# Kernel optimization log

Measured on AMD Instinct MI355X. Metric: run time of the kernel, lower is better.

The kernel has to match this reference:

```python
import jax, jax.numpy as jnp
import numpy as np

R, N, E = 3, 50000, 800000
IN, HID, HEADS, OUT = 128, 64, 2, 64


def setup_inputs() -> dict:
    key = jax.random.key(0)
    ks = jax.random.split(key, 12)
    s = 0.05
    return {
        "x": jax.random.normal(ks[0], (N, IN), jnp.float32),
        "src": jax.random.randint(ks[1], (R, E), 0, N, jnp.int32),
        "dst": jax.random.randint(ks[2], (R, E), 0, N, jnp.int32),
        "W1": jax.random.normal(ks[3], (R, IN, HEADS * HID), jnp.float32) * s,
        "al1": jax.random.normal(ks[4], (R, HEADS, HID), jnp.float32) * s,
        "ar1": jax.random.normal(ks[5], (R, HEADS, HID), jnp.float32) * s,
        "b1": jnp.zeros((R, HEADS * HID), jnp.float32),
        "W2": jax.random.normal(ks[6], (R, HEADS * HID, HID), jnp.float32) * s,
        "al2": jax.random.normal(ks[7], (R, 1, HID), jnp.float32) * s,
        "ar2": jax.random.normal(ks[8], (R, 1, HID), jnp.float32) * s,
        "b2": jnp.zeros((R, HID), jnp.float32),
        "Wl": jax.random.normal(ks[9], (HID, OUT), jnp.float32) * s,
        "bl": jnp.zeros((OUT,), jnp.float32),
    }


def gat_conv(x, src, dst, W, al, ar, b, heads, dim):
    """DGL GATConv on a homogeneous edge list: returns elu(aggregated) [N, heads, dim]."""
    n = x.shape[0]
    feat = (x @ W).reshape(n, heads, dim)                     # [N,H,D]
    el = (feat * al).sum(-1)                                  # [N,H]
    er = (feat * ar).sum(-1)                                  # [N,H]
    e = jax.nn.leaky_relu(el[src] + er[dst], 0.2)             # [E,H]
    # segment softmax over incoming edges of each dst node
    m = jax.lax.stop_gradient(jax.ops.segment_max(e, dst, num_segments=n))
    ee = jnp.exp(e - m[dst])                                  # [E,H]
    z = jax.ops.segment_sum(ee, dst, num_segments=n)          # [N,H]
    a = ee / z[dst]                                           # [E,H]
    msg = feat[src] * a[..., None]                            # [E,H,D]
    out = jax.ops.segment_sum(msg, dst, num_segments=n)       # [N,H,D]
    return jax.nn.elu(out + b.reshape(1, heads, dim))


def reference(x, src, dst, W1, al1, ar1, b1, W2, al2, ar2, b2, Wl, bl):
    # layer 1: per-relation GATConv, summed (HeteroGraphConv default aggregate='sum')
    h1 = sum(gat_conv(x, src[r], dst[r], W1[r], al1[r], ar1[r], b1[r], HEADS, HID)
             for r in range(R))                               # [N,H,HID]
    h1 = h1.reshape(N, HEADS * HID)                           # flatten(1)
    # layer 2: single-head GATConv per relation, summed
    h2 = sum(gat_conv(h1, src[r], dst[r], W2[r], al2[r], ar2[r], b2[r], 1, HID)
             for r in range(R))                               # [N,1,HID]
    h2 = h2.mean(1)                                           # mean over the single head
    return h2 @ Wl + bl                                       # [N,OUT]
```

## Files before the change

kernel.cpp:

```cpp
#include <hip/hip_runtime.h>

constexpr int R = 3;
constexpr int N = 50000;
constexpr int E = 800000;
constexpr int K = 128;
constexpr int NT16 = N / 16;
constexpr int GB = (NT16 + 3) / 4;

constexpr int BKT_SH = 9;
constexpr int NBKT = (N + 511) >> 9;
constexpr int BCAP = 10240;
constexpr int P1E = 4096;
constexpr int P1B = (E + P1E - 1) / P1E;

constexpr int NF1 = 192;
constexpr int NF2 = 96;
constexpr int NF3 = 16;
constexpr int PREP_BLKS = (NF1 + NF2 + NF3) / 4;

typedef __attribute__((ext_vector_type(8))) short bf16x8;
typedef __attribute__((ext_vector_type(4))) float f32x4;
typedef __attribute__((ext_vector_type(2))) float f32x2;


__device__ inline unsigned short f2bf(float f) {
    unsigned u = __float_as_uint(f);
    u += 0x7FFF + ((u >> 16) & 1);
    return (unsigned short)(u >> 16);
}
__device__ inline float bf2f_lo(unsigned p) { return __uint_as_float(p << 16); }
__device__ inline float bf2f_hi(unsigned p) { return __uint_as_float(p & 0xFFFF0000u); }

__device__ inline float lrelu02(float x) { return fmaxf(x, 0.2f * x); }
__device__ inline float elu1f(float x) { return x > 0.f ? x : __expf(x) - 1.f; }


__device__ void prep_frag(int f, int lane,
                          const float* __restrict__ W1, const float* __restrict__ W2,
                          const float* __restrict__ Wl,
                          short* __restrict__ WF1, short* __restrict__ WF2,
                          short* __restrict__ WF3) {
    int c = lane & 15, g = lane >> 4;
    const float* srcp;
    int stride;
    short* dstp;
    int hl;
    if (f < NF1) {
        hl = f & 1;
        int h = (f >> 1) & 1, ks = (f >> 2) & 3, tr = (f >> 4) & 3, r = f >> 6;
        int col = h * 64 + tr * 16 + c;
        srcp = W1 + (size_t)r * 128 * 128 + (size_t)(ks * 32 + g * 8) * 128 + col;
        stride = 128;
        dstp = WF1 + (size_t)f * 512 + lane * 8;
    } else if (f < NF1 + NF2) {
        int f2 = f - NF1;
        hl = f2 & 1;
        int ks = (f2 >> 1) & 3, t = f2 >> 3;
        int c192 = t * 16 + c;
        int r = c192 >> 6, col64 = c192 & 63;
        srcp = W2 + (size_t)r * 128 * 64 + (size_t)(ks * 32 + g * 8) * 64 + col64;
        stride = 64;
        dstp = WF2 + (size_t)f2 * 512 + lane * 8;
    } else {
        int f3 = f - NF1 - NF2;
        hl = f3 & 1;
        int ks = (f3 >> 1) & 1, t = f3 >> 2;
        srcp = Wl + (size_t)(ks * 32 + g * 8) * 64 + t * 16 + c;
        stride = 64;
        dstp = WF3 + (size_t)f3 * 512 + lane * 8;
    }
#pragma unroll
    for (int i = 0; i < 8; i++) {
        float v = srcp[(size_t)i * stride];
        unsigned short hi = f2bf(v);
        dstp[i] = hl ? (short)f2bf(v - __uint_as_float(((unsigned)hi) << 16)) : (short)hi;
    }
}

__global__ __launch_bounds__(256) void fusedA(const int* __restrict__ src,
                                              const int* __restrict__ dst,
                                              int* __restrict__ gcur,
                                              uint2* __restrict__ ebuf,
                                              const float* __restrict__ W1,
                                              const float* __restrict__ W2,
                                              const float* __restrict__ Wl,
                                              short* __restrict__ WF1,
                                              short* __restrict__ WF2,
                                              short* __restrict__ WF3) {
    __shared__ uint2 img[P1E];
    __shared__ int bins[NBKT], bstart[NBKT], gbase[NBKT];
    __shared__ int sc[128];
    const int tid = threadIdx.x;
    if (blockIdx.x < PREP_BLKS) {
        int f = blockIdx.x * 4 + (tid >> 6);
        prep_frag(f, tid & 63, W1, W2, Wl, WF1, WF2, WF3);
        return;
    }
    const int pbid = blockIdx.x - PREP_BLKS;
    const int r = pbid / P1B;
    const int e0 = (pbid % P1B) * P1E;
    const int cnt = min(P1E, E - e0);
    if (tid < NBKT) bins[tid] = 0;
    __syncthreads();
    int sv[16], dv[16], rk[16];
    int ni = 0;
    for (int i = tid; i < cnt; i += 256, ni++) {
        sv[ni] = src[(size_t)r * E + e0 + i];
        dv[ni] = dst[(size_t)r * E + e0 + i];
        rk[ni] = atomicAdd(&bins[dv[ni] >> BKT_SH], 1);
    }
    __syncthreads();
    if (tid < 128) sc[tid] = (tid < NBKT) ? bins[tid] : 0;
    __syncthreads();
    for (int off = 1; off < 128; off <<= 1) {
        int v = 0;
        if (tid < 128 && tid >= off) v = sc[tid - off];
        __syncthreads();
        if (tid < 128) sc[tid] += v;
        __syncthreads();
    }
    if (tid < NBKT) bstart[tid] = sc[tid] - bins[tid];
    __syncthreads();
    for (int j = 0; j < ni; j++) {
        int b = dv[j] >> BKT_SH;
        img[bstart[b] + rk[j]] = make_uint2((unsigned)sv[j], (unsigned)dv[j]);
    }
    if (tid < NBKT) gbase[tid] = bins[tid] ? atomicAdd(&gcur[r * NBKT + tid], bins[tid]) : 0;
    __syncthreads();
    for (int i = tid; i < cnt; i += 256) {
        uint2 e = img[i];
        int b = (int)(e.y >> BKT_SH);
        int pos = gbase[b] + (i - bstart[b]);
        if (pos < BCAP) ebuf[(size_t)(r * NBKT + b) * BCAP + pos] = e;
    }
}


__device__ inline void split_a_p(const float* __restrict__ xrow, bf16x8* ah, bf16x8* al) {
#pragma unroll
    for (int ks = 0; ks < 4; ks++) {
        f32x4 xa = *(const f32x4*)(xrow + ks * 32);
        f32x4 xb = *(const f32x4*)(xrow + ks * 32 + 4);
#pragma unroll
        for (int i = 0; i < 4; i++) {
            unsigned short h = f2bf(xa[i]);
            ah[ks][i] = (short)h;
            al[ks][i] = (short)f2bf(xa[i] - __uint_as_float(((unsigned)h) << 16));
            unsigned short h2 = f2bf(xb[i]);
            ah[ks][4 + i] = (short)h2;
            al[ks][4 + i] = (short)f2bf(xb[i] - __uint_as_float(((unsigned)h2) << 16));
        }
    }
}

__global__ __launch_bounds__(256) void fusedB(const uint2* __restrict__ ebuf,
                                              const int* __restrict__ gcur,
                                              int* __restrict__ rowptr,
                                              int* __restrict__ srclist,
                                              const float* __restrict__ X,
                                              const short* __restrict__ WF1,
                                              const float* __restrict__ al1,
                                              const float* __restrict__ ar1,
                                              unsigned* __restrict__ packed1,
                                              float* __restrict__ el,
                                              float* __restrict__ er) {
    alignas(16) __shared__ char smB[48128];
    __shared__ int gbase_s;
    const int tid = threadIdx.x;
    if (blockIdx.x < R * NBKT) {
        unsigned* img = (unsigned*)smB;
        int* bins = (int*)(smB + BCAP * 4);
        int* bst = bins + 512;
        int* cur = bst + 512;
        int* sc = cur + 512;
        const int r = blockIdx.x / NBKT, b = blockIdx.x % NBKT;
        const int bcnt = gcur[r * NBKT + b];
        const uint2* reg = ebuf + (size_t)(r * NBKT + b) * BCAP;
        for (int i = tid; i < 512; i += 256) bins[i] = 0;
        if (tid < 64) {
            int acc = 0;
            for (int base = 0; base < NBKT; base += 64) {
                int idx = base + tid;
                int v = (idx < b) ? gcur[r * NBKT + idx] : 0;
#pragma unroll
                for (int off = 32; off; off >>= 1) v += __shfl_xor(v, off);
                acc += v;
            }
            if (tid == 0) gbase_s = acc;
        }
        __syncthreads();
        const int gbase = gbase_s;
        for (int i = tid; i < bcnt; i += 256) atomicAdd(&bins[reg[i].y & 511], 1);
        __syncthreads();
        int v0 = bins[2 * tid], v1 = bins[2 * tid + 1];
        sc[tid] = v0 + v1;
        __syncthreads();
        for (int off = 1; off < 256; off <<= 1) {
            int t = 0;
            if (tid >= off) t = sc[tid - off];
            __syncthreads();
            sc[tid] += t;
            __syncthreads();
        }
        int base = sc[tid] - (v0 + v1);
        bst[2 * tid] = base;
        bst[2 * tid + 1] = base + v0;
        cur[2 * tid] = base;
        cur[2 * tid + 1] = base + v0;
        __syncthreads();
        for (int nl = tid; nl < 512; nl += 256) {
            int n = (b << BKT_SH) + nl;
            if (n < N) rowptr[r * (N + 1) + n] = gbase + bst[nl];
        }
        if (b == NBKT - 1 && tid == 0) rowptr[r * (N + 1) + N] = gbase + bcnt;
        for (int i = tid; i < bcnt; i += 256) {
            uint2 e = reg[i];
            int p = atomicAdd(&cur[e.y & 511], 1);
            img[p] = e.x;
        }
        __syncthreads();
        for (int i = tid; i < bcnt; i += 256) srclist[(size_t)r * E + gbase + i] = img[i];
        return;
    }
    float (*xs)[132] = (float(*)[132])smB;
    const int n0_blk = (blockIdx.x - R * NBKT) * 64;
    const int rows = min(64, N - n0_blk);
    for (int i = tid; i < rows * 32; i += 256) {
        int row = i >> 5, q4 = i & 31;
        *(f32x4*)&xs[row][q4 * 4] = *(const f32x4*)(X + (size_t)(n0_blk + row) * K + q4 * 4);
    }
    __syncthreads();
    const int lane = tid & 63;
    const int c = lane & 15;
    const int g = lane >> 4;
    const int n0 = n0_blk + (tid >> 6) * 16;
    if (n0 >= N) return;
    bf16x8 ah[4], al[4];
    split_a_p(&xs[(tid >> 6) * 16 + c][g * 8], ah, al);
    const bf16x8* fbase = (const bf16x8*)WF1 + lane;
    for (int r = 0; r < R; r++) {
        float pel0[4] = {0.f, 0.f, 0.f, 0.f}, per0[4] = {0.f, 0.f, 0.f, 0.f};
        float pel1[4] = {0.f, 0.f, 0.f, 0.f}, per1[4] = {0.f, 0.f, 0.f, 0.f};
        for (int tr = 0; tr < 4; tr++) {
            const bf16x8* fb = fbase + (size_t)((r * 4 + tr) * 16) * 64;
            f32x4 acc0 = {0.f, 0.f, 0.f, 0.f};
            f32x4 acc1 = {0.f, 0.f, 0.f, 0.f};
#pragma unroll
            for (int ks = 0; ks < 4; ks++) {
                bf16x8 b0h = fb[(ks * 4 + 0) * 64];
                bf16x8 b0l = fb[(ks * 4 + 1) * 64];
                bf16x8 b1h = fb[(ks * 4 + 2) * 64];
                bf16x8 b1l = fb[(ks * 4 + 3) * 64];
                acc0 = __builtin_amdgcn_mfma_f32_16x16x32_bf16(ah[ks], b0h, acc0, 0, 0, 0);
                acc0 = __builtin_amdgcn_mfma_f32_16x16x32_bf16(al[ks], b0h, acc0, 0, 0, 0);
                acc0 = __builtin_amdgcn_mfma_f32_16x16x32_bf16(ah[ks], b0l, acc0, 0, 0, 0);
                acc1 = __builtin_amdgcn_mfma_f32_16x16x32_bf16(ah[ks], b1h, acc1, 0, 0, 0);
                acc1 = __builtin_amdgcn_mfma_f32_16x16x32_bf16(al[ks], b1h, acc1, 0, 0, 0);
                acc1 = __builtin_amdgcn_mfma_f32_16x16x32_bf16(ah[ks], b1l, acc1, 0, 0, 0);
            }
            float a0 = al1[r * 128 + tr * 16 + c];
            float r0 = ar1[r * 128 + tr * 16 + c];
            float a1 = al1[r * 128 + 64 + tr * 16 + c];
            float r1 = ar1[r * 128 + 64 + tr * 16 + c];
#pragma unroll
            for (int i = 0; i < 4; i++) {
                pel0[i] += acc0[i] * a0;
                per0[i] += acc0[i] * r0;
                pel1[i] += acc1[i] * a1;
                per1[i] += acc1[i] * r1;
                int m = g * 4 + i;
                unsigned wrd = (unsigned)f2bf(acc0[i]) | ((unsigned)f2bf(acc1[i]) << 16);
                packed1[(size_t)(n0 + m) * 192 + r * 64 + tr * 16 + c] = wrd;
            }
        }
#pragma unroll
        for (int off = 1; off < 16; off <<= 1) {
#pragma unroll
            for (int i = 0; i < 4; i++) {
                pel0[i] += __shfl_xor(pel0[i], off);
                per0[i] += __shfl_xor(per0[i], off);
                pel1[i] += __shfl_xor(pel1[i], off);
                per1[i] += __shfl_xor(per1[i], off);
            }
        }
        if (c == 0) {
#pragma unroll
            for (int i = 0; i < 4; i++) {
                int n = n0 + g * 4 + i;
                el[(r * N + n) * 2 + 0] = pel0[i];
                el[(r * N + n) * 2 + 1] = pel1[i];
                er[(r * N + n) * 2 + 0] = per0[i];
                er[(r * N + n) * 2 + 1] = per1[i];
            }
        }
    }
}


__global__ __launch_bounds__(256) void gemm2_mfma(const float* __restrict__ X,
                                                  const short* __restrict__ WF2,
                                                  const float* __restrict__ al2,
                                                  const float* __restrict__ ar2,
                                                  unsigned short* __restrict__ packed2,
                                                  float* __restrict__ el,
                                                  float* __restrict__ er) {
    __shared__ float xs[64][132];
    const int n0_blk = blockIdx.x * 64;
    const int tid = threadIdx.x;
    const int rows = min(64, N - n0_blk);
    for (int i = tid; i < rows * 32; i += 256) {
        int row = i >> 5, q4 = i & 31;
        *(f32x4*)&xs[row][q4 * 4] = *(const f32x4*)(X + (size_t)(n0_blk + row) * K + q4 * 4);
    }
    __syncthreads();
    const int lane = tid & 63;
    const int c = lane & 15;
    const int g = lane >> 4;
    const int n0 = n0_blk + (tid >> 6) * 16;
    if (n0 >= N) return;
    bf16x8 ah[4], al[4];
    split_a_p(&xs[(tid >> 6) * 16 + c][g * 8], ah, al);
    const bf16x8* fbase = (const bf16x8*)WF2 + lane;
    float pel[4], per[4];
    for (int t = 0; t < 12; t++) {
        int r = t >> 2, tt = t & 3;
        if (tt == 0) {
#pragma unroll
            for (int i = 0; i < 4; i++) { pel[i] = 0.f; per[i] = 0.f; }
        }
        f32x4 acc = {0.f, 0.f, 0.f, 0.f};
#pragma unroll
        for (int ks = 0; ks < 4; ks++) {
            bf16x8 vh = fbase[(size_t)((t * 4 + ks) * 2 + 0) * 64];
            bf16x8 vl = fbase[(size_t)((t * 4 + ks) * 2 + 1) * 64];
            acc = __builtin_amdgcn_mfma_f32_16x16x32_bf16(ah[ks], vh, acc, 0, 0, 0);
            acc = __builtin_amdgcn_mfma_f32_16x16x32_bf16(al[ks], vh, acc, 0, 0, 0);
            acc = __builtin_amdgcn_mfma_f32_16x16x32_bf16(ah[ks], vl, acc, 0, 0, 0);
        }
        float a = al2[r * 64 + tt * 16 + c];
        float rr = ar2[r * 64 + tt * 16 + c];
#pragma unroll
        for (int i = 0; i < 4; i++) {
            pel[i] += acc[i] * a;
            per[i] += acc[i] * rr;
            int m = g * 4 + i;
            packed2[(size_t)(n0 + m) * 192 + t * 16 + c] = f2bf(acc[i]);
        }
        if (tt == 3) {
#pragma unroll
            for (int off = 1; off < 16; off <<= 1) {
#pragma unroll
                for (int i = 0; i < 4; i++) {
                    pel[i] += __shfl_xor(pel[i], off);
                    per[i] += __shfl_xor(per[i], off);
                }
            }
            if (c == 0) {
#pragma unroll
                for (int i = 0; i < 4; i++) {
                    int n = n0 + g * 4 + i;
                    el[r * N + n] = pel[i];
                    er[r * N + n] = per[i];
                }
            }
        }
    }
}


__global__ __launch_bounds__(256) void agg_l1(const char* __restrict__ packed1b,
                                              const float* __restrict__ el_,
                                              const float* __restrict__ er_,
                                              const int* __restrict__ rowptr,
                                              const int* __restrict__ srclist,
                                              const float* __restrict__ b1,
                                              float* __restrict__ h1) {
    int n = (blockIdx.x * blockDim.x + threadIdx.x) >> 6;
    int lane = threadIdx.x & 63;
    if (n >= N) return;
    const int q = lane >> 4;
    const int c = lane & 15;
    const unsigned coff = (unsigned)(c * 16);
    const float2* el2 = (const float2*)el_;
    const float2* er2 = (const float2*)er_;
    float hacc0[4] = {0.f, 0.f, 0.f, 0.f}, hacc1[4] = {0.f, 0.f, 0.f, 0.f};
    for (int r = 0; r < R; r++) {
        int beg = rowptr[r * (N + 1) + n];
        int end = rowptr[r * (N + 1) + n + 1];
        float2 ern = er2[r * N + n];
        const int* sl = srclist + r * E;
        const int rbase = r * N;
        const unsigned robf = (unsigned)(r * 256);
        f32x2 acc2[4] = {{0.f, 0.f}, {0.f, 0.f}, {0.f, 0.f}, {0.f, 0.f}};
        float zl0 = 0.f, zl1 = 0.f;
        for (int cbeg = beg; cbeg < end; cbeg += 64) {
            int cnt = min(64, end - cbeg);
            unsigned ofs = 0;
            float ew0 = 0.f, ew1 = 0.f;
            if (lane < cnt) {
                int sid = sl[cbeg + lane];
                float2 e = el2[rbase + sid];
                ew0 = __expf(lrelu02(e.x + ern.x));
                ew1 = __expf(lrelu02(e.y + ern.y));
                ofs = (unsigned)sid * 768u + robf;
            }
            zl0 += ew0;
            zl1 += ew1;
            int kmax = (cnt + 3) & ~3;
            int k = 0;
            for (; k + 8 <= kmax; k += 8) {
                int iA = k + q, iB = k + 4 + q;
                unsigned oA = (unsigned)__shfl((int)ofs, iA);
                unsigned oB = (unsigned)__shfl((int)ofs, iB);
                f32x2 wA = {__shfl(ew0, iA), __shfl(ew1, iA)};
                f32x2 wB = {__shfl(ew0, iB), __shfl(ew1, iB)};
                uint4 vA = *(const uint4*)(packed1b + (oA + coff));
                uint4 vB = *(const uint4*)(packed1b + (oB + coff));
                acc2[0] += (f32x2){bf2f_lo(vA.x), bf2f_hi(vA.x)} * wA;
                acc2[1] += (f32x2){bf2f_lo(vA.y), bf2f_hi(vA.y)} * wA;
                acc2[2] += (f32x2){bf2f_lo(vA.z), bf2f_hi(vA.z)} * wA;
                acc2[3] += (f32x2){bf2f_lo(vA.w), bf2f_hi(vA.w)} * wA;
                acc2[0] += (f32x2){bf2f_lo(vB.x), bf2f_hi(vB.x)} * wB;
                acc2[1] += (f32x2){bf2f_lo(vB.y), bf2f_hi(vB.y)} * wB;
                acc2[2] += (f32x2){bf2f_lo(vB.z), bf2f_hi(vB.z)} * wB;
                acc2[3] += (f32x2){bf2f_lo(vB.w), bf2f_hi(vB.w)} * wB;
            }
            if (k < kmax) {
                int idx = k + q;
                unsigned o = (unsigned)__shfl((int)ofs, idx);
                f32x2 w = {__shfl(ew0, idx), __shfl(ew1, idx)};
                uint4 v = *(const uint4*)(packed1b + (o + coff));
                acc2[0] += (f32x2){bf2f_lo(v.x), bf2f_hi(v.x)} * w;
                acc2[1] += (f32x2){bf2f_lo(v.y), bf2f_hi(v.y)} * w;
                acc2[2] += (f32x2){bf2f_lo(v.z), bf2f_hi(v.z)} * w;
                acc2[3] += (f32x2){bf2f_lo(v.w), bf2f_hi(v.w)} * w;
            }
        }
#pragma unroll
        for (int i = 0; i < 4; i++) {
            acc2[i].x += __shfl_xor(acc2[i].x, 16);
            acc2[i].x += __shfl_xor(acc2[i].x, 32);
            acc2[i].y += __shfl_xor(acc2[i].y, 16);
            acc2[i].y += __shfl_xor(acc2[i].y, 32);
        }
#pragma unroll
        for (int off = 32; off; off >>= 1) {
            zl0 += __shfl_xor(zl0, off);
            zl1 += __shfl_xor(zl1, off);
        }
        float rz0 = (end > beg) ? __builtin_amdgcn_rcpf(zl0) : 0.f;
        float rz1 = (end > beg) ? __builtin_amdgcn_rcpf(zl1) : 0.f;
        float4 bv0 = *(const float4*)(b1 + r * 128 + c * 4);
        float4 bv1 = *(const float4*)(b1 + r * 128 + 64 + c * 4);
        hacc0[0] += elu1f(acc2[0].x * rz0 + bv0.x);
        hacc0[1] += elu1f(acc2[1].x * rz0 + bv0.y);
        hacc0[2] += elu1f(acc2[2].x * rz0 + bv0.z);
        hacc0[3] += elu1f(acc2[3].x * rz0 + bv0.w);
        hacc1[0] += elu1f(acc2[0].y * rz1 + bv1.x);
        hacc1[1] += elu1f(acc2[1].y * rz1 + bv1.y);
        hacc1[2] += elu1f(acc2[2].y * rz1 + bv1.z);
        hacc1[3] += elu1f(acc2[3].y * rz1 + bv1.w);
    }
    if (q == 0) {
        float4 o0 = {hacc0[0], hacc0[1], hacc0[2], hacc0[3]};
        float4 o1 = {hacc1[0], hacc1[1], hacc1[2], hacc1[3]};
        *(float4*)(h1 + (size_t)n * 128 + c * 4) = o0;
        *(float4*)(h1 + (size_t)n * 128 + 64 + c * 4) = o1;
    }
}

__global__ __launch_bounds__(256) void agg_l2(const char* __restrict__ packed2b,
                                              const float* __restrict__ el,
                                              const float* __restrict__ er,
                                              const int* __restrict__ rowptr,
                                              const int* __restrict__ srclist,
                                              const float* __restrict__ b2,
                                              float* __restrict__ h2) {
    int n = (blockIdx.x * blockDim.x + threadIdx.x) >> 6;
    int lane = threadIdx.x & 63;
    if (n >= N) return;
    const int q = lane >> 4;
    const int c = lane & 15;
    const unsigned coff = (unsigned)(c * 8);
    float hacc[4] = {0.f, 0.f, 0.f, 0.f};
    for (int r = 0; r < R; r++) {
        int beg = rowptr[r * (N + 1) + n];
        int end = rowptr[r * (N + 1) + n + 1];
        float ern = er[r * N + n];
        const int* sl = srclist + r * E;
        const int rbase = r * N;
        const unsigned robf = (unsigned)(r * 128);
        f32x2 acc01 = {0.f, 0.f}, acc23 = {0.f, 0.f};
        float zl = 0.f;
        for (int cbeg = beg; cbeg < end; cbeg += 64) {
            int cnt = min(64, end - cbeg);
            unsigned ofs = 0;
            float ew = 0.f;
            if (lane < cnt) {
                int sid = sl[cbeg + lane];
                ew = __expf(lrelu02(el[rbase + sid] + ern));
                ofs = (unsigned)sid * 384u + robf;
            }
            zl += ew;
            int kmax = (cnt + 3) & ~3;
            int k = 0;
            for (; k + 8 <= kmax; k += 8) {
                int iA = k + q, iB = k + 4 + q;
                unsigned oA = (unsigned)__shfl((int)ofs, iA);
                unsigned oB = (unsigned)__shfl((int)ofs, iB);
                float aA = __shfl(ew, iA), aB = __shfl(ew, iB);
                uint2 vA = *(const uint2*)(packed2b + (oA + coff));
                uint2 vB = *(const uint2*)(packed2b + (oB + coff));
                f32x2 wA = {aA, aA}, wB = {aB, aB};
                acc01 += (f32x2){bf2f_lo(vA.x), bf2f_hi(vA.x)} * wA;
                acc23 += (f32x2){bf2f_lo(vA.y), bf2f_hi(vA.y)} * wA;
                acc01 += (f32x2){bf2f_lo(vB.x), bf2f_hi(vB.x)} * wB;
                acc23 += (f32x2){bf2f_lo(vB.y), bf2f_hi(vB.y)} * wB;
            }
            if (k < kmax) {
                int idx = k + q;
                unsigned o = (unsigned)__shfl((int)ofs, idx);
                float a = __shfl(ew, idx);
                uint2 v = *(const uint2*)(packed2b + (o + coff));
                f32x2 w = {a, a};
                acc01 += (f32x2){bf2f_lo(v.x), bf2f_hi(v.x)} * w;
                acc23 += (f32x2){bf2f_lo(v.y), bf2f_hi(v.y)} * w;
            }
        }
        acc01.x += __shfl_xor(acc01.x, 16); acc01.x += __shfl_xor(acc01.x, 32);
        acc01.y += __shfl_xor(acc01.y, 16); acc01.y += __shfl_xor(acc01.y, 32);
        acc23.x += __shfl_xor(acc23.x, 16); acc23.x += __shfl_xor(acc23.x, 32);
        acc23.y += __shfl_xor(acc23.y, 16); acc23.y += __shfl_xor(acc23.y, 32);
#pragma unroll
        for (int off = 32; off; off >>= 1) zl += __shfl_xor(zl, off);
        float rz = (end > beg) ? __builtin_amdgcn_rcpf(zl) : 0.f;
        float4 bv = *(const float4*)(b2 + r * 64 + c * 4);
        hacc[0] += elu1f(acc01.x * rz + bv.x);
        hacc[1] += elu1f(acc01.y * rz + bv.y);
        hacc[2] += elu1f(acc23.x * rz + bv.z);
        hacc[3] += elu1f(acc23.y * rz + bv.w);
    }
    if (q == 0) {
        float4 o = {hacc[0], hacc[1], hacc[2], hacc[3]};
        *(float4*)(h2 + (size_t)n * 64 + c * 4) = o;
    }
}


__global__ __launch_bounds__(256) void gemm3_mfma(const float* __restrict__ h2,
                                                  const short* __restrict__ WF3,
                                                  const float* __restrict__ bl,
                                                  float* __restrict__ out) {
    __shared__ float xs[64][68];
    const int n0_blk = blockIdx.x * 64;
    const int tid = threadIdx.x;
    const int rows = min(64, N - n0_blk);
    for (int i = tid; i < rows * 16; i += 256) {
        int row = i >> 4, q4 = i & 15;
        *(f32x4*)&xs[row][q4 * 4] = *(const f32x4*)(h2 + (size_t)(n0_blk + row) * 64 + q4 * 4);
    }
    __syncthreads();
    const int lane = tid & 63;
    const int c = lane & 15;
    const int g = lane >> 4;
    const int n0 = n0_blk + (tid >> 6) * 16;
    if (n0 >= N) return;
    bf16x8 ah[2], al[2];
    const float* xrow = &xs[(tid >> 6) * 16 + c][g * 8];
#pragma unroll
    for (int ks = 0; ks < 2; ks++) {
        f32x4 xa = *(const f32x4*)(xrow + ks * 32);
        f32x4 xb = *(const f32x4*)(xrow + ks * 32 + 4);
#pragma unroll
        for (int i = 0; i < 4; i++) {
            unsigned short h = f2bf(xa[i]);
            ah[ks][i] = (short)h;
            al[ks][i] = (short)f2bf(xa[i] - __uint_as_float(((unsigned)h) << 16));
            unsigned short h2v = f2bf(xb[i]);
            ah[ks][4 + i] = (short)h2v;
            al[ks][4 + i] = (short)f2bf(xb[i] - __uint_as_float(((unsigned)h2v) << 16));
        }
    }
    const bf16x8* fbase = (const bf16x8*)WF3 + lane;
    for (int t = 0; t < 4; t++) {
        f32x4 acc = {0.f, 0.f, 0.f, 0.f};
#pragma unroll
        for (int ks = 0; ks < 2; ks++) {
            bf16x8 vh = fbase[((t * 2 + ks) * 2 + 0) * 64];
            bf16x8 vl = fbase[((t * 2 + ks) * 2 + 1) * 64];
            acc = __builtin_amdgcn_mfma_f32_16x16x32_bf16(ah[ks], vh, acc, 0, 0, 0);
            acc = __builtin_amdgcn_mfma_f32_16x16x32_bf16(al[ks], vh, acc, 0, 0, 0);
            acc = __builtin_amdgcn_mfma_f32_16x16x32_bf16(ah[ks], vl, acc, 0, 0, 0);
        }
        float bb = bl[t * 16 + c];
#pragma unroll
        for (int i = 0; i < 4; i++) {
            out[(size_t)(n0 + g * 4 + i) * 64 + t * 16 + c] = acc[i] + bb;
        }
    }
}


extern "C" void kernel_launch(void* const* d_in, const int* in_sizes, int n_in,
                              void* d_out, int out_size, void* d_ws, size_t ws_size,
                              hipStream_t stream) {
    const float* x   = (const float*)d_in[0];
    const int*   src = (const int*)d_in[1];
    const int*   dst = (const int*)d_in[2];
    const float* W1  = (const float*)d_in[3];
    const float* al1 = (const float*)d_in[4];
    const float* ar1 = (const float*)d_in[5];
    const float* b1  = (const float*)d_in[6];
    const float* W2  = (const float*)d_in[7];
    const float* al2 = (const float*)d_in[8];
    const float* ar2 = (const float*)d_in[9];
    const float* b2  = (const float*)d_in[10];
    const float* Wl  = (const float*)d_in[11];
    const float* bl  = (const float*)d_in[12];
    float* out = (float*)d_out;

    char* ws = (char*)d_ws;
    size_t off = 0;
    auto alloc = [&](size_t bytes) {
        char* p = ws + off;
        off += (bytes + 255) & ~(size_t)255;
        return p;
    };
    unsigned*       packed1 = (unsigned*)alloc(sizeof(unsigned) * (size_t)N * R * 64);
    unsigned short* packed2 = (unsigned short*)alloc(sizeof(unsigned short) * (size_t)N * R * 64);
    float* h1      = (float*)alloc(sizeof(float) * (size_t)N * 128);
    float* h2      = (float*)alloc(sizeof(float) * (size_t)N * 64);
    float* el1     = (float*)alloc(sizeof(float) * (size_t)R * N * 2);
    float* er1     = (float*)alloc(sizeof(float) * (size_t)R * N * 2);
    float* el2     = (float*)alloc(sizeof(float) * (size_t)R * N);
    float* er2     = (float*)alloc(sizeof(float) * (size_t)R * N);
    int*   rowptr  = (int*)alloc(sizeof(int) * (size_t)R * (N + 1));
    int*   srclist = (int*)alloc(sizeof(int) * (size_t)R * E);
    uint2* ebuf    = (uint2*)alloc(sizeof(uint2) * (size_t)R * NBKT * BCAP);
    int*   gcur    = (int*)alloc(sizeof(int) * (size_t)R * NBKT);
    short* WF1     = (short*)alloc(sizeof(short) * (size_t)NF1 * 512);
    short* WF2     = (short*)alloc(sizeof(short) * (size_t)NF2 * 512);
    short* WF3     = (short*)alloc(sizeof(short) * (size_t)NF3 * 512);

    hipMemsetAsync(gcur, 0, sizeof(int) * (size_t)R * NBKT, stream);

    fusedA<<<PREP_BLKS + R * P1B, 256, 0, stream>>>(src, dst, gcur, ebuf,
                                                    W1, W2, Wl, WF1, WF2, WF3);

    fusedB<<<R * NBKT + GB, 256, 0, stream>>>(ebuf, gcur, rowptr, srclist,
                                              x, WF1, al1, ar1, packed1, el1, er1);

    agg_l1<<<(N * 64 + 255) / 256, 256, 0, stream>>>((const char*)packed1, el1, er1,
                                                     rowptr, srclist, b1, h1);

    gemm2_mfma<<<GB, 256, 0, stream>>>(h1, WF2, al2, ar2, packed2, el2, er2);
    agg_l2<<<(N * 64 + 255) / 256, 256, 0, stream>>>((const char*)packed2, el2, er2,
                                                     rowptr, srclist, b2, h2);

    gemm3_mfma<<<GB, 256, 0, stream>>>(h2, WF3, bl, out);
}
```

Measured before the change: 277.5 us.

## Pack edge records into 32 bits and fuse layer-2 aggregation with final GEMM

Edge bucket records shrink from 8 bytes to 4 by packing the bucket id, a 16-bit source index and the low 9 bits of dst into one word. This halves ebuf traffic between the two bucketing kernels. The layer-2 aggregation is fused with the output projection: each 1024-thread block aggregates 16 nodes into shared memory, then one wave runs the MFMA GEMM, so h2 never goes to global memory and one launch is saved. Risks are src indices needing 16 bits (50000 fits) and the GEMM stage using only one wave per block.

After: 280.8 us. About the same (+1.2%).

```diff
diff --git a/kernel.cpp b/kernel.cpp
--- a/kernel.cpp
+++ b/kernel.cpp
@@ -80,14 +80,14 @@
 __global__ __launch_bounds__(256) void fusedA(const int* __restrict__ src,
                                               const int* __restrict__ dst,
                                               int* __restrict__ gcur,
-                                              uint2* __restrict__ ebuf,
+                                              unsigned* __restrict__ ebuf,
                                               const float* __restrict__ W1,
                                               const float* __restrict__ W2,
                                               const float* __restrict__ Wl,
                                               short* __restrict__ WF1,
                                               short* __restrict__ WF2,
                                               short* __restrict__ WF3) {
-    __shared__ uint2 img[P1E];
+    __shared__ unsigned img[P1E];
     __shared__ int bins[NBKT], bstart[NBKT], gbase[NBKT];
     __shared__ int sc[128];
     const int tid = threadIdx.x;
@@ -123,13 +123,14 @@
     __syncthreads();
     for (int j = 0; j < ni; j++) {
         int b = dv[j] >> BKT_SH;
-        img[bstart[b] + rk[j]] = make_uint2((unsigned)sv[j], (unsigned)dv[j]);
+        img[bstart[b] + rk[j]] = ((unsigned)b << 25) | ((unsigned)sv[j] << 9) |
+                                 ((unsigned)dv[j] & 511u);
     }
     if (tid < NBKT) gbase[tid] = bins[tid] ? atomicAdd(&gcur[r * NBKT + tid], bins[tid]) : 0;
     __syncthreads();
     for (int i = tid; i < cnt; i += 256) {
-        uint2 e = img[i];
-        int b = (int)(e.y >> BKT_SH);
+        unsigned e = img[i];
+        int b = (int)(e >> 25);
         int pos = gbase[b] + (i - bstart[b]);
         if (pos < BCAP) ebuf[(size_t)(r * NBKT + b) * BCAP + pos] = e;
     }
@@ -153,7 +154,7 @@
     }
 }
 
-__global__ __launch_bounds__(256) void fusedB(const uint2* __restrict__ ebuf,
+__global__ __launch_bounds__(256) void fusedB(const unsigned* __restrict__ ebuf,
                                               const int* __restrict__ gcur,
                                               int* __restrict__ rowptr,
                                               int* __restrict__ srclist,
@@ -175,7 +176,7 @@
         int* sc = cur + 512;
         const int r = blockIdx.x / NBKT, b = blockIdx.x % NBKT;
         const int bcnt = gcur[r * NBKT + b];
-        const uint2* reg = ebuf + (size_t)(r * NBKT + b) * BCAP;
+        const unsigned* reg = ebuf + (size_t)(r * NBKT + b) * BCAP;
         for (int i = tid; i < 512; i += 256) bins[i] = 0;
         if (tid < 64) {
             int acc = 0;
@@ -190,7 +191,7 @@
         }
         __syncthreads();
         const int gbase = gbase_s;
-        for (int i = tid; i < bcnt; i += 256) atomicAdd(&bins[reg[i].y & 511], 1);
+        for (int i = tid; i < bcnt; i += 256) atomicAdd(&bins[reg[i] & 511u], 1);
         __syncthreads();
         int v0 = bins[2 * tid], v1 = bins[2 * tid + 1];
         sc[tid] = v0 + v1;
@@ -214,12 +215,12 @@
         }
         if (b == NBKT - 1 && tid == 0) rowptr[r * (N + 1) + N] = gbase + bcnt;
         for (int i = tid; i < bcnt; i += 256) {
-            uint2 e = reg[i];
-            int p = atomicAdd(&cur[e.y & 511], 1);
-            img[p] = e.x;
+            unsigned e = reg[i];
+            int p = atomicAdd(&cur[e & 511u], 1);
+            img[p] = (e >> 9) & 0xFFFFu;
         }
         __syncthreads();
-        for (int i = tid; i < bcnt; i += 256) srclist[(size_t)r * E + gbase + i] = img[i];
+        for (int i = tid; i < bcnt; i += 256) srclist[(size_t)r * E + gbase + i] = (int)img[i];
         return;
     }
     float (*xs)[132] = (float(*)[132])smB;
@@ -469,16 +470,21 @@
     }
 }
 
-__global__ __launch_bounds__(256) void agg_l2(const char* __restrict__ packed2b,
-                                              const float* __restrict__ el,
-                                              const float* __restrict__ er,
-                                              const int* __restrict__ rowptr,
-                                              const int* __restrict__ srclist,
-                                              const float* __restrict__ b2,
-                                              float* __restrict__ h2) {
-    int n = (blockIdx.x * blockDim.x + threadIdx.x) >> 6;
-    int lane = threadIdx.x & 63;
-    if (n >= N) return;
+
+__global__ __launch_bounds__(1024) void agg_l2_gemm3(const char* __restrict__ packed2b,
+                                                     const float* __restrict__ el,
+                                                     const float* __restrict__ er,
+                                                     const int* __restrict__ rowptr,
+                                                     const int* __restrict__ srclist,
+                                                     const float* __restrict__ b2,
+                                                     const short* __restrict__ WF3,
+                                                     const float* __restrict__ bl,
+                                                     float* __restrict__ out) {
+    __shared__ float hs[16][68];
+    const int tid = threadIdx.x;
+    const int w = tid >> 6;
+    const int lane = tid & 63;
+    const int n = blockIdx.x * 16 + w;
     const int q = lane >> 4;
     const int c = lane & 15;
     const unsigned coff = (unsigned)(c * 8);
@@ -522,9 +528,9 @@
                 unsigned o = (unsigned)__shfl((int)ofs, idx);
                 float a = __shfl(ew, idx);
                 uint2 v = *(const uint2*)(packed2b + (o + coff));
-                f32x2 w = {a, a};
-                acc01 += (f32x2){bf2f_lo(v.x), bf2f_hi(v.x)} * w;
-                acc23 += (f32x2){bf2f_lo(v.y), bf2f_hi(v.y)} * w;
+                f32x2 ww = {a, a};
+                acc01 += (f32x2){bf2f_lo(v.x), bf2f_hi(v.x)} * ww;
+                acc23 += (f32x2){bf2f_lo(v.y), bf2f_hi(v.y)} * ww;
             }
         }
         acc01.x += __shfl_xor(acc01.x, 16); acc01.x += __shfl_xor(acc01.x, 32);
@@ -541,32 +547,17 @@
         hacc[3] += elu1f(acc23.y * rz + bv.w);
     }
     if (q == 0) {
-        float4 o = {hacc[0], hacc[1], hacc[2], hacc[3]};
-        *(float4*)(h2 + (size_t)n * 64 + c * 4) = o;
-    }
-}
-
-
-__global__ __launch_bounds__(256) void gemm3_mfma(const float* __restrict__ h2,
-                                                  const short* __restrict__ WF3,
-                                                  const float* __restrict__ bl,
-                                                  float* __restrict__ out) {
-    __shared__ float xs[64][68];
-    const int n0_blk = blockIdx.x * 64;
-    const int tid = threadIdx.x;
-    const int rows = min(64, N - n0_blk);
-    for (int i = tid; i < rows * 16; i += 256) {
-        int row = i >> 4, q4 = i & 15;
-        *(f32x4*)&xs[row][q4 * 4] = *(const f32x4*)(h2 + (size_t)(n0_blk + row) * 64 + q4 * 4);
-    }
-    __syncthreads();
-    const int lane = tid & 63;
-    const int c = lane & 15;
-    const int g = lane >> 4;
-    const int n0 = n0_blk + (tid >> 6) * 16;
-    if (n0 >= N) return;
+        hs[w][c * 4 + 0] = hacc[0];
+        hs[w][c * 4 + 1] = hacc[1];
+        hs[w][c * 4 + 2] = hacc[2];
+        hs[w][c * 4 + 3] = hacc[3];
+    }
+    __syncthreads();
+    if (w != 0) return;
+    const int g = q;
+    const int n0 = blockIdx.x * 16;
     bf16x8 ah[2], al[2];
-    const float* xrow = &xs[(tid >> 6) * 16 + c][g * 8];
+    const float* xrow = &hs[c][g * 8];
 #pragma unroll
     for (int ks = 0; ks < 2; ks++) {
         f32x4 xa = *(const f32x4*)(xrow + ks * 32);
@@ -629,14 +620,13 @@
     unsigned*       packed1 = (unsigned*)alloc(sizeof(unsigned) * (size_t)N * R * 64);
     unsigned short* packed2 = (unsigned short*)alloc(sizeof(unsigned short) * (size_t)N * R * 64);
     float* h1      = (float*)alloc(sizeof(float) * (size_t)N * 128);
-    float* h2      = (float*)alloc(sizeof(float) * (size_t)N * 64);
     float* el1     = (float*)alloc(sizeof(float) * (size_t)R * N * 2);
     float* er1     = (float*)alloc(sizeof(float) * (size_t)R * N * 2);
     float* el2     = (float*)alloc(sizeof(float) * (size_t)R * N);
     float* er2     = (float*)alloc(sizeof(float) * (size_t)R * N);
     int*   rowptr  = (int*)alloc(sizeof(int) * (size_t)R * (N + 1));
     int*   srclist = (int*)alloc(sizeof(int) * (size_t)R * E);
-    uint2* ebuf    = (uint2*)alloc(sizeof(uint2) * (size_t)R * NBKT * BCAP);
+    unsigned* ebuf = (unsigned*)alloc(sizeof(unsigned) * (size_t)R * NBKT * BCAP);
     int*   gcur    = (int*)alloc(sizeof(int) * (size_t)R * NBKT);
     short* WF1     = (short*)alloc(sizeof(short) * (size_t)NF1 * 512);
     short* WF2     = (short*)alloc(sizeof(short) * (size_t)NF2 * 512);
@@ -654,8 +644,7 @@
                                                      rowptr, srclist, b1, h1);
 
     gemm2_mfma<<<GB, 256, 0, stream>>>(h1, WF2, al2, ar2, packed2, el2, er2);
-    agg_l2<<<(N * 64 + 255) / 256, 256, 0, stream>>>((const char*)packed2, el2, er2,
-                                                     rowptr, srclist, b2, h2);
-
-    gemm3_mfma<<<GB, 256, 0, stream>>>(h2, WF3, bl, out);
-}
+
+    agg_l2_gemm3<<<NT16, 1024, 0, stream>>>((const char*)packed2, el2, er2,
+                                            rowptr, srclist, b2, WF3, bl, out);
+}
```
